# Kernel optimization log

Measured on AMD Instinct MI355X. Metric: run time of the kernel, lower is better.

The kernel has to match this reference:

```python
import jax, jax.numpy as jnp
import numpy as np

N = 50000   # nodes
E = 800000  # edges
F = 64      # node_feature_dim
H = 128     # hidden_dim


def setup_inputs() -> dict:
    key = jax.random.key(0)
    ks = jax.random.split(key, 20)
    def w(k, shape, fan_in):
        return jax.random.normal(k, shape, jnp.float32) / np.sqrt(fan_in)
    return {
        "x": jax.random.normal(ks[0], (N, F), jnp.float32),
        "edge_index": jax.random.randint(ks[1], (2, E), 0, N, jnp.int32),
        "enc_w1": w(ks[2], (F, H), F), "enc_b1": jnp.zeros((H,), jnp.float32),
        "enc_w2": w(ks[3], (H, H), H), "enc_b2": jnp.zeros((H,), jnp.float32),
        "w_c1": w(ks[4], (H, H), H), "b_c1": jnp.zeros((H,), jnp.float32),
        "w_c2": w(ks[5], (H, H), H), "b_c2": jnp.zeros((H,), jnp.float32),
        "w_c3": w(ks[6], (H, H), H), "b_c3": jnp.zeros((H,), jnp.float32),
        "dec_w1": w(ks[7], (H, H), H), "dec_b1": jnp.zeros((H,), jnp.float32),
        "dec_w2": w(ks[8], (H, F), H), "dec_b2": jnp.zeros((F,), jnp.float32),
    }


def _gcn_conv(h, W, b, src, dst, dinv):
    # PyG GCNConv: D^-1/2 (A+I) D^-1/2 (h W) + b  (self-loops already in src/dst)
    hw = h @ W                                   # [N, H]
    norm = dinv[src] * dinv[dst]                 # [E+N]
    msg = hw[src] * norm[:, None]                # gather + scale
    return jax.ops.segment_sum(msg, dst, num_segments=N) + b


def reference(x, edge_index, enc_w1, enc_b1, enc_w2, enc_b2,
              w_c1, b_c1, w_c2, b_c2, w_c3, b_c3,
              dec_w1, dec_b1, dec_w2, dec_b2):
    loop = jnp.arange(N, dtype=edge_index.dtype)
    src = jnp.concatenate([edge_index[0], loop])
    dst = jnp.concatenate([edge_index[1], loop])
    deg = jax.ops.segment_sum(jnp.ones_like(dst, jnp.float32), dst, num_segments=N)
    dinv = jax.lax.rsqrt(deg)  # deg >= 1 because of self-loops

    h = jax.nn.relu(x @ enc_w1 + enc_b1) @ enc_w2 + enc_b2  # encoder MLP
    h = jax.nn.relu(_gcn_conv(h, w_c1, b_c1, src, dst, dinv))
    h = jax.nn.relu(_gcn_conv(h, w_c2, b_c2, src, dst, dinv))
    h = jax.nn.relu(_gcn_conv(h, w_c3, b_c3, src, dst, dinv))
    # window_size == 1: chunk+cat is identity
    out = jax.nn.relu(h @ dec_w1 + dec_b1) @ dec_w2 + dec_b2  # decoder MLP
    return jax.nn.sigmoid(out)
```

## Files before the change

### kernel.cpp

```cpp
#include <hip/hip_runtime.h>
#include <stdint.h>

#define NN 50000
#define NE 800000
#define FD 64
#define HD 128
#define NBKT 196
#define BCAP 5120

typedef __attribute__((ext_vector_type(8))) short short8;
typedef __attribute__((ext_vector_type(4))) float f32x4;

#define AS1 __attribute__((address_space(1)))
#define AS3 __attribute__((address_space(3)))

__device__ __forceinline__ float bflo(unsigned int v) {
    union { unsigned int u; float f; } c; c.u = v << 16; return c.f;
}
__device__ __forceinline__ float bfhi(unsigned int v) {
    union { unsigned int u; float f; } c; c.u = v & 0xffff0000u; return c.f;
}
__device__ __forceinline__ unsigned short f2bf(float f) {
    union { float f; unsigned int u; } c; c.f = f;
    unsigned int u = c.u;
    return (unsigned short)((u + 0x7fffu + ((u >> 16) & 1u)) >> 16);
}
__device__ __forceinline__ unsigned int pack2(float a, float b) {
    return (unsigned int)f2bf(a) | ((unsigned int)f2bf(b) << 16);
}

__global__ void wt_k(const float* __restrict__ w0, const float* __restrict__ w1,
                     const float* __restrict__ w2, const float* __restrict__ w3,
                     const float* __restrict__ w4, const float* __restrict__ w5,
                     const float* __restrict__ w6,
                     unsigned short* __restrict__ t0, unsigned short* __restrict__ t1,
                     unsigned short* __restrict__ t2, unsigned short* __restrict__ t3,
                     unsigned short* __restrict__ t4, unsigned short* __restrict__ t5,
                     unsigned short* __restrict__ t6)
{
    int b = blockIdx.x;
    const float* W; unsigned short* T; int K, C;
    if      (b <  32) { W = w0; T = t0; K =  64; C = 128; }
    else if (b <  96) { W = w1; T = t1; K = 128; C = 128; b -= 32; }
    else if (b < 160) { W = w2; T = t2; K = 128; C = 128; b -= 96; }
    else if (b < 224) { W = w3; T = t3; K = 128; C = 128; b -= 160; }
    else if (b < 288) { W = w4; T = t4; K = 128; C = 128; b -= 224; }
    else if (b < 352) { W = w5; T = t5; K = 128; C = 128; b -= 288; }
    else              { W = w6; T = t6; K = 128; C =  64; b -= 352; }
    int e = b * 256 + threadIdx.x;
    int k, c;
    if (C == 128) { k = e >> 7; c = e & 127; } else { k = e >> 6; c = e & 63; }
    int gmask = (K >> 3) - 1;
    int gsw = (k >> 3) ^ (c & gmask);
    T[c * K + gsw * 8 + (k & 7)] = f2bf(W[e]);
}

__global__ void scanB_k(int* __restrict__ bsum, int nb) {
    __shared__ int sh[256];
    int t = threadIdx.x;
    int v = (t < nb) ? bsum[t] : 0;
    sh[t] = v; __syncthreads();
    for (int d = 1; d < 256; d <<= 1) {
        int x = (t >= d) ? sh[t - d] : 0; __syncthreads();
        sh[t] += x; __syncthreads();
    }
    if (t < nb) bsum[t] = sh[t] - v;
}

template <int K, int COLS, int EPI, bool BIAS, bool RSCALE, bool A_F32, bool OUT_F32>
__device__ __forceinline__ void mgemm_dev(
    int bid,
    const void* __restrict__ Av,
    const unsigned short* __restrict__ Wt,
    const float* __restrict__ bias,
    const float* __restrict__ dinv,
    void* __restrict__ outv, int nrows)
{
    constexpr int NB = COLS / 16;
    constexpr int KC = K / 32;
    constexpr int GMASK = (K >> 3) - 1;
    __shared__ __align__(16) unsigned char Ws8[COLS * K * 2];

    const int tid = threadIdx.x;
    const int wave = tid >> 6;
    const int lane = tid & 63;

    {
        constexpr int ROUNDS = COLS * K * 2 / 4096;
        const int gb = wave * 1024 + lane * 16;
        const int lb = wave * 1024;
        #pragma unroll
        for (int r = 0; r < ROUNDS; r++) {
            __builtin_amdgcn_global_load_lds(
                (const AS1 unsigned int*)((const unsigned char*)Wt + r * 4096 + gb),
                (AS3 unsigned int*)(Ws8 + r * 4096 + lb),
                16, 0, 0);
        }
    }

    const int m = lane & 15;
    const int q = lane >> 4;
    const int row0 = bid * 64 + wave * 16;

    f32x4 acc[NB];
    #pragma unroll
    for (int i = 0; i < NB; i++) acc[i] = (f32x4){0.f, 0.f, 0.f, 0.f};

    const bool arow_ok = !A_F32 || (row0 + m) < nrows;

    short8 af[KC];
    #pragma unroll
    for (int kc = 0; kc < KC; kc++) {
        if constexpr (A_F32) {
            const float* arowf = (const float*)Av + (size_t)(row0 + m) * K + q * 8 + kc * 32;
            float4 lo = make_float4(0.f, 0.f, 0.f, 0.f), hi = lo;
            if (arow_ok) { lo = *(const float4*)arowf; hi = *(const float4*)(arowf + 4); }
            af[kc][0] = (short)f2bf(lo.x); af[kc][1] = (short)f2bf(lo.y);
            af[kc][2] = (short)f2bf(lo.z); af[kc][3] = (short)f2bf(lo.w);
            af[kc][4] = (short)f2bf(hi.x); af[kc][5] = (short)f2bf(hi.y);
            af[kc][6] = (short)f2bf(hi.z); af[kc][7] = (short)f2bf(hi.w);
        } else {
            const unsigned short* arow = (const unsigned short*)Av + (size_t)(row0 + m) * K + q * 8 + kc * 32;
            af[kc] = *(const short8*)arow;
        }
    }
    __syncthreads();

    #pragma unroll
    for (int kc = 0; kc < KC; kc++) {
        #pragma unroll
        for (int nb = 0; nb < NB; nb++) {
            const int c = nb * 16 + m;
            const int gsw = (kc * 4 + q) ^ (c & GMASK);
            short8 bf = *(const short8*)&Ws8[(c * K + gsw * 8) * 2];
            acc[nb] = __builtin_amdgcn_mfma_f32_16x16x32_bf16(af[kc], bf, acc[nb], 0, 0, 0);
        }
    }

    float bv[NB];
    #pragma unroll
    for (int nb = 0; nb < NB; nb++) bv[nb] = BIAS ? bias[nb * 16 + m] : 0.f;

    #pragma unroll
    for (int r = 0; r < 4; r++) {
        int row = row0 + q * 4 + r;
        if (row < nrows) {
            float sc = RSCALE ? dinv[row] : 1.f;
            #pragma unroll
            for (int nb = 0; nb < NB; nb++) {
                float t = acc[nb][r];
                if (RSCALE) t *= sc;
                t += bv[nb];
                if (EPI == 1) t = fmaxf(t, 0.f);
                if (EPI == 2) t = 1.f / (1.f + __expf(-t));
                if constexpr (OUT_F32) {
                    ((float*)outv)[(size_t)row * COLS + nb * 16 + m] = t;
                } else {
                    ((unsigned short*)outv)[(size_t)row * COLS + nb * 16 + m] = f2bf(t);
                }
            }
        }
    }
}

template <int K, int COLS, int EPI, bool BIAS, bool RSCALE, bool A_F32, bool OUT_F32>
__global__ __launch_bounds__(256) void mgemm_k(
    const void* __restrict__ Av, const unsigned short* __restrict__ Wt,
    const float* __restrict__ bias, const float* __restrict__ dinv,
    void* __restrict__ outv, int nrows)
{
    mgemm_dev<K, COLS, EPI, BIAS, RSCALE, A_F32, OUT_F32>(blockIdx.x, Av, Wt, bias, dinv, outv, nrows);
}

__global__ __launch_bounds__(256) void k1_k(
    const float* __restrict__ x, const unsigned short* __restrict__ t0,
    const float* __restrict__ enc_b1, unsigned short* __restrict__ bufA,
    const int* __restrict__ src, const int* __restrict__ dst,
    int* __restrict__ cnt, int* __restrict__ gcnt,
    unsigned int* __restrict__ bucket, int gb)
{
    if ((int)blockIdx.x < gb) {
        mgemm_dev<64, 128, 1, true, false, true, false>(blockIdx.x, x, t0, enc_b1, nullptr, bufA, NN);
    } else {
        __shared__ int lcnt[NBKT], lofs[NBKT];
        const int tid = threadIdx.x;
        const int bb = blockIdx.x - gb;
        if (tid < NBKT) lcnt[tid] = 0;
        __syncthreads();
        unsigned int ent[8];
        #pragma unroll
        for (int u = 0; u < 8; u++) {
            int g = bb * 2048 + u * 256 + tid;
            if (g < NE) {
                int d = dst[g], s = src[g];
                atomicAdd(&cnt[d], 1);
                int bk = d >> 8;
                atomicAdd(&lcnt[bk], 1);
                ent[u] = (unsigned int)s | ((unsigned int)(d & 255) << 16)
                       | ((unsigned int)bk << 24);
            } else ent[u] = 0xFFFFFFFFu;
        }
        __syncthreads();
        if (tid < NBKT) lofs[tid] = atomicAdd(&gcnt[tid], lcnt[tid]);
        __syncthreads();
        #pragma unroll
        for (int u = 0; u < 8; u++) {
            if (ent[u] != 0xFFFFFFFFu) {
                int bk = ent[u] >> 24;
                int r = atomicAdd(&lofs[bk], 1);
                bucket[bk * BCAP + r] = ent[u];
            }
        }
    }
}

__global__ __launch_bounds__(256) void k2_k(
    const unsigned short* __restrict__ bufA, const unsigned short* __restrict__ t1,
    const float* __restrict__ enc_b2, unsigned short* __restrict__ bufB,
    const int* __restrict__ cnt, int* __restrict__ off, int* __restrict__ bsum,
    float* __restrict__ dinv, int gb)
{
    if ((int)blockIdx.x < gb) {
        mgemm_dev<128, 128, 0, true, false, false, false>(blockIdx.x, bufA, t1, enc_b2, nullptr, bufB, NN);
    } else {
        __shared__ int sh[256];
        int t = threadIdx.x;
        int g = (blockIdx.x - gb) * 256 + t;
        int v = (g < NN) ? cnt[g] : 0;
        if (g < NN) dinv[g] = rsqrtf((float)(v + 1));
        sh[t] = v; __syncthreads();
        for (int d = 1; d < 256; d <<= 1) {
            int x2 = (t >= d) ? sh[t - d] : 0; __syncthreads();
            sh[t] += x2; __syncthreads();
        }
        if (g < NN) off[g] = sh[t] - v;
        if (t == 255) bsum[blockIdx.x - gb] = sh[255];
    }
}

__global__ __launch_bounds__(256) void k4_k(
    const unsigned short* __restrict__ bufB, const unsigned short* __restrict__ t2,
    const float* __restrict__ dinv, unsigned short* __restrict__ bufA,
    const int* __restrict__ gcnt, const unsigned int* __restrict__ bucket,
    const int* __restrict__ off, const int* __restrict__ bsum,
    unsigned short* __restrict__ csr, int gb)
{
    if ((int)blockIdx.x < gb) {
        mgemm_dev<128, 128, 0, false, true, false, false>(blockIdx.x, bufB, t2, nullptr, dinv, bufA, NN);
    } else {
        __shared__ int lc[256];
        const int tid = threadIdx.x;
        const int b = blockIdx.x - gb;
        lc[tid] = 0;
        __syncthreads();
        const int cb = gcnt[b];
        const int base = bsum[b];
        for (int i = tid; i < cb; i += 256) {
            unsigned int e = bucket[b * BCAP + i];
            int s = e & 0xffff;
            int dl = (e >> 16) & 255;
            int r = atomicAdd(&lc[dl], 1);
            csr[off[b * 256 + dl] + base + r] = (unsigned short)s;
        }
    }
}

__global__ __launch_bounds__(256) void agg_k(
    const uint2* __restrict__ hws,
    const int* __restrict__ off, const int* __restrict__ bsum,
    const unsigned short* __restrict__ csr,
    const float* __restrict__ dinv, const float* __restrict__ bias,
    uint2* __restrict__ out, int n)
{
    int node = blockIdx.x * 8 + (threadIdx.x >> 5);
    if (node >= n) return;
    int lane = threadIdx.x & 31;

    uint2 v = hws[node * 32 + lane];
    float s0 = bflo(v.x), s1 = bfhi(v.x), s2 = bflo(v.y), s3 = bfhi(v.y);

    int b = off[node] + bsum[node >> 8];
    int e = (node + 1 < n) ? (off[node + 1] + bsum[(node + 1) >> 8]) : NE;
    int j = b;
    for (; j + 8 <= e; j += 8) {
        uint2 t[8];
        #pragma unroll
        for (int u = 0; u < 8; u++) t[u] = hws[(int)csr[j + u] * 32 + lane];
        #pragma unroll
        for (int u = 0; u < 8; u++) {
            s0 += bflo(t[u].x); s1 += bfhi(t[u].x);
            s2 += bflo(t[u].y); s3 += bfhi(t[u].y);
        }
    }
    for (; j < e; j++) {
        uint2 t = hws[(int)csr[j] * 32 + lane];
        s0 += bflo(t.x); s1 += bfhi(t.x);
        s2 += bflo(t.y); s3 += bfhi(t.y);
    }

    float di = dinv[node];
    float4 bv = *(const float4*)(bias + 4 * lane);
    float r0 = fmaxf(fmaf(di, s0, bv.x), 0.f);
    float r1 = fmaxf(fmaf(di, s1, bv.y), 0.f);
    float r2 = fmaxf(fmaf(di, s2, bv.z), 0.f);
    float r3 = fmaxf(fmaf(di, s3, bv.w), 0.f);
    uint2 o; o.x = pack2(r0, r1); o.y = pack2(r2, r3);
    out[node * 32 + lane] = o;
}

extern "C" void kernel_launch(void* const* d_in, const int* in_sizes, int n_in,
                              void* d_out, int out_size, void* d_ws, size_t ws_size,
                              hipStream_t stream)
{
    const float* x      = (const float*)d_in[0];
    const int*   ei     = (const int*)d_in[1];
    const float* enc_w1 = (const float*)d_in[2];
    const float* enc_b1 = (const float*)d_in[3];
    const float* enc_w2 = (const float*)d_in[4];
    const float* enc_b2 = (const float*)d_in[5];
    const float* w_c1   = (const float*)d_in[6];
    const float* b_c1   = (const float*)d_in[7];
    const float* w_c2   = (const float*)d_in[8];
    const float* b_c2   = (const float*)d_in[9];
    const float* w_c3   = (const float*)d_in[10];
    const float* b_c3   = (const float*)d_in[11];
    const float* dec_w1 = (const float*)d_in[12];
    const float* dec_b1 = (const float*)d_in[13];
    const float* dec_w2 = (const float*)d_in[14];
    const float* dec_b2 = (const float*)d_in[15];

    const int* src = ei;
    const int* dst = ei + NE;

    const int NP = 50048;

    char* ws = (char*)d_ws;
    size_t o = 0;
    auto alloc = [&](size_t bytes) -> void* {
        void* p = ws + o;
        o = (o + bytes + 255) & ~(size_t)255;
        return p;
    };
    int*   cnt  = (int*)alloc((size_t)NN * 4);
    int*   gcnt = (int*)alloc(256 * 4);
    int*   off  = (int*)alloc((size_t)(NN + 1) * 4);
    int*   bsum = (int*)alloc(256 * 4);
    unsigned short* csr = (unsigned short*)alloc((size_t)NE * 2);
    unsigned int* bucket = (unsigned int*)alloc((size_t)NBKT * BCAP * 4);
    float* dinv = (float*)alloc((size_t)NN * 4);
    unsigned short* bufA = (unsigned short*)alloc((size_t)NP * HD * 2);
    unsigned short* bufB = (unsigned short*)alloc((size_t)NP * HD * 2);
    unsigned short* t0 = (unsigned short*)alloc(64 * 128 * 2);
    unsigned short* t1 = (unsigned short*)alloc(128 * 128 * 2);
    unsigned short* t2 = (unsigned short*)alloc(128 * 128 * 2);
    unsigned short* t3 = (unsigned short*)alloc(128 * 128 * 2);
    unsigned short* t4 = (unsigned short*)alloc(128 * 128 * 2);
    unsigned short* t5 = (unsigned short*)alloc(128 * 128 * 2);
    unsigned short* t6 = (unsigned short*)alloc(128 * 64 * 2);
    (void)ws_size; (void)n_in; (void)in_sizes; (void)out_size;

    hipMemsetAsync(cnt, 0, (size_t)((char*)gcnt - (char*)cnt) + 256 * 4, stream);

    const int PB = (NE + 2047) / 2048;
    const int NB_ = (NN + 255) / 256;
    const int GB = NP / 64;
    const int AB = (NN + 7) / 8;

    wt_k<<<384, 256, 0, stream>>>(enc_w1, enc_w2, w_c1, w_c2, w_c3, dec_w1, dec_w2,
                                  t0, t1, t2, t3, t4, t5, t6);
    k1_k<<<GB + PB, 256, 0, stream>>>(x, t0, enc_b1, bufA, src, dst, cnt, gcnt, bucket, GB);
    k2_k<<<GB + NB_, 256, 0, stream>>>(bufA, t1, enc_b2, bufB, cnt, off, bsum, dinv, GB);
    scanB_k<<<1, 256, 0, stream>>>(bsum, NB_);
    k4_k<<<GB + NBKT, 256, 0, stream>>>(bufB, t2, dinv, bufA, gcnt, bucket, off, bsum, csr, GB);

    agg_k<<<AB, 256, 0, stream>>>((const uint2*)bufA, off, bsum, csr, dinv, b_c1, (uint2*)bufB, NN);
    mgemm_k<128, 128, 0, false, true, false, false><<<GB, 256, 0, stream>>>(bufB, t3, nullptr, dinv, bufA, NN);
    agg_k<<<AB, 256, 0, stream>>>((const uint2*)bufA, off, bsum, csr, dinv, b_c2, (uint2*)bufB, NN);
    mgemm_k<128, 128, 0, false, true, false, false><<<GB, 256, 0, stream>>>(bufB, t4, nullptr, dinv, bufA, NN);
    agg_k<<<AB, 256, 0, stream>>>((const uint2*)bufA, off, bsum, csr, dinv, b_c3, (uint2*)bufB, NN);
    mgemm_k<128, 128, 1, true, false, false, false><<<GB, 256, 0, stream>>>(bufB, t5, dec_b1, nullptr, bufA, NN);
    mgemm_k<128, 64, 2, true, false, false, true><<<GB, 256, 0, stream>>>(bufA, t6, dec_b2, nullptr, d_out, NN);
}
```

Baseline: 311.1 us.

## Build CSR from buckets without global degree atomics, stage bucket writes in LDS

Drops the per-edge global atomicAdd on node degree counts. Per-node counts, dinv and local offsets are now derived inside each bucket block, which counts its own edges in shared memory. The bucket-partition pass now handles 4096 edges per block and stages entries in LDS sorted by bucket, so the global bucket writes are contiguous runs instead of scattered single stores. The pipeline is reordered: scanB runs over the bucket totals, then one fused kernel builds the CSR alongside the second encoder GEMM. The first conv GEMM becomes its own launch, since dinv is only ready after the CSR kernel, which adds a launch and removes overlap for that GEMM.

After: 281.1 us. 9.7% less time.

```diff
diff --git a/kernel.cpp b/kernel.cpp
--- a/kernel.cpp
+++ b/kernel.cpp
@@ -7,6 +7,7 @@
 #define HD 128
 #define NBKT 196
 #define BCAP 5120
+#define P1E 4096
 
 typedef __attribute__((ext_vector_type(8))) short short8;
 typedef __attribute__((ext_vector_type(4))) float f32x4;
@@ -55,10 +56,10 @@
     T[c * K + gsw * 8 + (k & 7)] = f2bf(W[e]);
 }
 
-__global__ void scanB_k(int* __restrict__ bsum, int nb) {
+__global__ void scanB_k(const int* __restrict__ gcnt, int* __restrict__ bsum, int nb) {
     __shared__ int sh[256];
     int t = threadIdx.x;
-    int v = (t < nb) ? bsum[t] : 0;
+    int v = (t < nb) ? gcnt[t] : 0;
     sh[t] = v; __syncthreads();
     for (int d = 1; d < 256; d <<= 1) {
         int x = (t >= d) ? sh[t - d] : 0; __syncthreads();
@@ -176,24 +177,23 @@
     const float* __restrict__ x, const unsigned short* __restrict__ t0,
     const float* __restrict__ enc_b1, unsigned short* __restrict__ bufA,
     const int* __restrict__ src, const int* __restrict__ dst,
-    int* __restrict__ cnt, int* __restrict__ gcnt,
-    unsigned int* __restrict__ bucket, int gb)
+    int* __restrict__ gcnt, unsigned int* __restrict__ bucket, int gb)
 {
     if ((int)blockIdx.x < gb) {
         mgemm_dev<64, 128, 1, true, false, true, false>(blockIdx.x, x, t0, enc_b1, nullptr, bufA, NN);
     } else {
-        __shared__ int lcnt[NBKT], lofs[NBKT];
+        __shared__ int lcnt[256], lsw[256], lexc[256], lofs[256], lrank[256];
+        __shared__ unsigned int stage[P1E];
         const int tid = threadIdx.x;
         const int bb = blockIdx.x - gb;
-        if (tid < NBKT) lcnt[tid] = 0;
-        __syncthreads();
-        unsigned int ent[8];
-        #pragma unroll
-        for (int u = 0; u < 8; u++) {
-            int g = bb * 2048 + u * 256 + tid;
+        lcnt[tid] = 0; lrank[tid] = 0;
+        __syncthreads();
+        unsigned int ent[P1E / 256];
+        #pragma unroll
+        for (int u = 0; u < P1E / 256; u++) {
+            int g = bb * P1E + u * 256 + tid;
             if (g < NE) {
                 int d = dst[g], s = src[g];
-                atomicAdd(&cnt[d], 1);
                 int bk = d >> 8;
                 atomicAdd(&lcnt[bk], 1);
                 ent[u] = (unsigned int)s | ((unsigned int)(d & 255) << 16)
@@ -201,15 +201,29 @@
             } else ent[u] = 0xFFFFFFFFu;
         }
         __syncthreads();
-        if (tid < NBKT) lofs[tid] = atomicAdd(&gcnt[tid], lcnt[tid]);
-        __syncthreads();
-        #pragma unroll
-        for (int u = 0; u < 8; u++) {
+        int v = lcnt[tid];
+        lsw[tid] = v; __syncthreads();
+        for (int d = 1; d < 256; d <<= 1) {
+            int xx = (tid >= d) ? lsw[tid - d] : 0; __syncthreads();
+            lsw[tid] += xx; __syncthreads();
+        }
+        lexc[tid] = lsw[tid] - v;
+        lofs[tid] = (v > 0) ? atomicAdd(&gcnt[tid], v) : 0;
+        __syncthreads();
+        #pragma unroll
+        for (int u = 0; u < P1E / 256; u++) {
             if (ent[u] != 0xFFFFFFFFu) {
                 int bk = ent[u] >> 24;
-                int r = atomicAdd(&lofs[bk], 1);
-                bucket[bk * BCAP + r] = ent[u];
+                int r = atomicAdd(&lrank[bk], 1);
+                stage[lexc[bk] + r] = ent[u];
             }
+        }
+        __syncthreads();
+        int cb = NE - bb * P1E; if (cb > P1E) cb = P1E;
+        for (int i = tid; i < cb; i += 256) {
+            unsigned int e = stage[i];
+            int bk = e >> 24;
+            bucket[(size_t)bk * BCAP + lofs[bk] + (i - lexc[bk])] = e;
         }
     }
 }
@@ -217,50 +231,49 @@
 __global__ __launch_bounds__(256) void k2_k(
     const unsigned short* __restrict__ bufA, const unsigned short* __restrict__ t1,
     const float* __restrict__ enc_b2, unsigned short* __restrict__ bufB,
-    const int* __restrict__ cnt, int* __restrict__ off, int* __restrict__ bsum,
-    float* __restrict__ dinv, int gb)
+    const int* __restrict__ gcnt, const unsigned int* __restrict__ bucket,
+    const int* __restrict__ bsum,
+    int* __restrict__ off, float* __restrict__ dinv,
+    unsigned short* __restrict__ csr, int gb)
 {
     if ((int)blockIdx.x < gb) {
         mgemm_dev<128, 128, 0, true, false, false, false>(blockIdx.x, bufA, t1, enc_b2, nullptr, bufB, NN);
     } else {
-        __shared__ int sh[256];
-        int t = threadIdx.x;
-        int g = (blockIdx.x - gb) * 256 + t;
-        int v = (g < NN) ? cnt[g] : 0;
-        if (g < NN) dinv[g] = rsqrtf((float)(v + 1));
-        sh[t] = v; __syncthreads();
-        for (int d = 1; d < 256; d <<= 1) {
-            int x2 = (t >= d) ? sh[t - d] : 0; __syncthreads();
-            sh[t] += x2; __syncthreads();
-        }
-        if (g < NN) off[g] = sh[t] - v;
-        if (t == 255) bsum[blockIdx.x - gb] = sh[255];
-    }
-}
-
-__global__ __launch_bounds__(256) void k4_k(
-    const unsigned short* __restrict__ bufB, const unsigned short* __restrict__ t2,
-    const float* __restrict__ dinv, unsigned short* __restrict__ bufA,
-    const int* __restrict__ gcnt, const unsigned int* __restrict__ bucket,
-    const int* __restrict__ off, const int* __restrict__ bsum,
-    unsigned short* __restrict__ csr, int gb)
-{
-    if ((int)blockIdx.x < gb) {
-        mgemm_dev<128, 128, 0, false, true, false, false>(blockIdx.x, bufB, t2, nullptr, dinv, bufA, NN);
-    } else {
-        __shared__ int lc[256];
+        __shared__ int lc[256], sw[256], sexc[256], lr[256];
         const int tid = threadIdx.x;
         const int b = blockIdx.x - gb;
-        lc[tid] = 0;
-        __syncthreads();
         const int cb = gcnt[b];
+        unsigned int ent[BCAP / 256];
+        #pragma unroll
+        for (int u = 0; u < BCAP / 256; u++) {
+            int i = u * 256 + tid;
+            ent[u] = (i < cb) ? bucket[(size_t)b * BCAP + i] : 0xFFFFFFFFu;
+        }
+        lc[tid] = 0; lr[tid] = 0;
+        __syncthreads();
+        #pragma unroll
+        for (int u = 0; u < BCAP / 256; u++)
+            if (ent[u] != 0xFFFFFFFFu) atomicAdd(&lc[(ent[u] >> 16) & 255], 1);
+        __syncthreads();
+        int v = lc[tid];
+        int node = b * 256 + tid;
+        if (node < NN) dinv[node] = rsqrtf((float)(v + 1));
+        sw[tid] = v; __syncthreads();
+        for (int d = 1; d < 256; d <<= 1) {
+            int xx = (tid >= d) ? sw[tid - d] : 0; __syncthreads();
+            sw[tid] += xx; __syncthreads();
+        }
+        sexc[tid] = sw[tid] - v;
+        if (node < NN) off[node] = sexc[tid];
+        __syncthreads();
         const int base = bsum[b];
-        for (int i = tid; i < cb; i += 256) {
-            unsigned int e = bucket[b * BCAP + i];
-            int s = e & 0xffff;
-            int dl = (e >> 16) & 255;
-            int r = atomicAdd(&lc[dl], 1);
-            csr[off[b * 256 + dl] + base + r] = (unsigned short)s;
+        #pragma unroll
+        for (int u = 0; u < BCAP / 256; u++) {
+            if (ent[u] != 0xFFFFFFFFu) {
+                int dl = (ent[u] >> 16) & 255;
+                int r = atomicAdd(&lr[dl], 1);
+                csr[base + sexc[dl] + r] = (unsigned short)(ent[u] & 0xffff);
+            }
         }
     }
 }
@@ -341,7 +354,6 @@
         o = (o + bytes + 255) & ~(size_t)255;
         return p;
     };
-    int*   cnt  = (int*)alloc((size_t)NN * 4);
     int*   gcnt = (int*)alloc(256 * 4);
     int*   off  = (int*)alloc((size_t)(NN + 1) * 4);
     int*   bsum = (int*)alloc(256 * 4);
@@ -359,20 +371,19 @@
     unsigned short* t6 = (unsigned short*)alloc(128 * 64 * 2);
     (void)ws_size; (void)n_in; (void)in_sizes; (void)out_size;
 
-    hipMemsetAsync(cnt, 0, (size_t)((char*)gcnt - (char*)cnt) + 256 * 4, stream);
-
-    const int PB = (NE + 2047) / 2048;
-    const int NB_ = (NN + 255) / 256;
+    hipMemsetAsync(gcnt, 0, 256 * 4, stream);
+
+    const int PB = (NE + P1E - 1) / P1E;
     const int GB = NP / 64;
     const int AB = (NN + 7) / 8;
 
     wt_k<<<384, 256, 0, stream>>>(enc_w1, enc_w2, w_c1, w_c2, w_c3, dec_w1, dec_w2,
                                   t0, t1, t2, t3, t4, t5, t6);
-    k1_k<<<GB + PB, 256, 0, stream>>>(x, t0, enc_b1, bufA, src, dst, cnt, gcnt, bucket, GB);
-    k2_k<<<GB + NB_, 256, 0, stream>>>(bufA, t1, enc_b2, bufB, cnt, off, bsum, dinv, GB);
-    scanB_k<<<1, 256, 0, stream>>>(bsum, NB_);
-    k4_k<<<GB + NBKT, 256, 0, stream>>>(bufB, t2, dinv, bufA, gcnt, bucket, off, bsum, csr, GB);
-
+    k1_k<<<GB + PB, 256, 0, stream>>>(x, t0, enc_b1, bufA, src, dst, gcnt, bucket, GB);
+    scanB_k<<<1, 256, 0, stream>>>(gcnt, bsum, NBKT);
+    k2_k<<<GB + NBKT, 256, 0, stream>>>(bufA, t1, enc_b2, bufB, gcnt, bucket, bsum,
+                                        off, dinv, csr, GB);
+    mgemm_k<128, 128, 0, false, true, false, false><<<GB, 256, 0, stream>>>(bufB, t2, nullptr, dinv, bufA, NN);
     agg_k<<<AB, 256, 0, stream>>>((const uint2*)bufA, off, bsum, csr, dinv, b_c1, (uint2*)bufB, NN);
     mgemm_k<128, 128, 0, false, true, false, false><<<GB, 256, 0, stream>>>(bufB, t3, nullptr, dinv, bufA, NN);
     agg_k<<<AB, 256, 0, stream>>>((const uint2*)bufA, off, bsum, csr, dinv, b_c2, (uint2*)bufB, NN);
```
